# Optimization experiments

Measured on AMD Instinct MI355X. Metric: run time of the kernel, lower is better.

## Reference

```python
import jax, jax.numpy as jnp
import numpy as np

B = 32768      # batch
N_IN = 128     # input nodes
L = 8          # topological layers
W = 256        # nodes per layer
K = 16         # fan-in per node


def setup_inputs() -> dict:
    key = jax.random.key(0)
    k_x, k_w, k_b, k_e = jax.random.split(key, 4)
    inputs = jax.random.normal(k_x, (B, N_IN), dtype=jnp.float32)
    # scale weights down so sigmoid isn't saturated with fan-in 16
    weights = jax.random.normal(k_w, (L, W, K), dtype=jnp.float32) * 0.25
    biases = jax.random.normal(k_b, (L, W), dtype=jnp.float32) * 0.1
    # DAG-valid edges: layer l may only gather from the N_IN + l*W already-computed nodes
    ek = jax.random.split(k_e, L)
    edge_idx = jnp.stack([
        jax.random.randint(ek[l], (W, K), 0, N_IN + l * W, dtype=jnp.int32)
        for l in range(L)
    ])  # [L, W, K]
    return {"inputs": inputs, "weights": weights, "biases": biases,
            "edge_idx": edge_idx}


def reference(inputs, weights, biases, edge_idx):
    # values buffer starts as the input-node activations: [B, N_IN]
    vals = inputs
    n_layers = weights.shape[0]
    for l in range(n_layers):
        gathered = vals[:, edge_idx[l]]                      # [B, W, K] per-node gather
        pre = jnp.einsum('bwk,wk->bw', gathered, weights[l]) + biases[l]
        vals = jnp.concatenate([vals, jax.nn.sigmoid(pre)], axis=1)
    # output nodes are the last layer, concatenated in order
    return vals[:, -W:]
```

## Files before the change

kernel.cpp:

```cpp
#include <hip/hip_runtime.h>
#include <hip/hip_bf16.h>
#include <hip/hip_fp16.h>


#define NB   32768
#define NIN  128
#define NL   8
#define NW   256
#define NK   16
#define RPB  8
#define STORED (NIN + (NL - 1) * NW)

typedef _Float16 h2 __attribute__((ext_vector_type(2)));
typedef __fp16   fp16v2 __attribute__((ext_vector_type(2)));

__device__ __forceinline__ unsigned pk16(float a, float b) {
    fp16v2 p = __builtin_amdgcn_cvt_pkrtz(a, b);
    return __builtin_bit_cast(unsigned, p);
}

__device__ __forceinline__ void fma_feat(float acc[RPB], float w, uint4 p) {
    const h2 h0 = __builtin_bit_cast(h2, p.x);
    const h2 h1 = __builtin_bit_cast(h2, p.y);
    const h2 h2v = __builtin_bit_cast(h2, p.z);
    const h2 h3 = __builtin_bit_cast(h2, p.w);
    acc[0] = fmaf((float)h0[0], w, acc[0]);
    acc[1] = fmaf((float)h0[1], w, acc[1]);
    acc[2] = fmaf((float)h1[0], w, acc[2]);
    acc[3] = fmaf((float)h1[1], w, acc[3]);
    acc[4] = fmaf((float)h2v[0], w, acc[4]);
    acc[5] = fmaf((float)h2v[1], w, acc[5]);
    acc[6] = fmaf((float)h3[0], w, acc[6]);
    acc[7] = fmaf((float)h3[1], w, acc[7]);
}

__global__ __launch_bounds__(256, 5)
void ffn_gather_kernel(const float* __restrict__ inputs,
                       const float* __restrict__ weights,
                       const float* __restrict__ biases,
                       const int*   __restrict__ edge_idx,
                       float* __restrict__ out)
{
    __shared__ uint4 vals[STORED];

    const int t = threadIdx.x;
    const long long row0 = (long long)blockIdx.x * RPB;

    if (t < NIN) {
        float v[RPB];
        #pragma unroll
        for (int r = 0; r < RPB; ++r) v[r] = inputs[(row0 + r) * NIN + t];
        uint4 p;
        p.x = pk16(v[0], v[1]);
        p.y = pk16(v[2], v[3]);
        p.z = pk16(v[4], v[5]);
        p.w = pk16(v[6], v[7]);
        vals[t] = p;
    }
    __syncthreads();

    #pragma unroll
    for (int l = 0; l < NL; ++l) {
        const int base = (l * NW + t) * NK;
        const int4*   iq = (const int4*)(edge_idx + base);
        const float4* wq = (const float4*)(weights + base);

        const float b = biases[l * NW + t];
        float acc[RPB];
        #pragma unroll
        for (int r = 0; r < RPB; ++r) acc[r] = b;

        #pragma unroll
        for (int kk = 0; kk < NK / 4; ++kk) {
            const int4   i4 = iq[kk];
            const float4 w4 = wq[kk];
            const uint4 p0 = vals[i4.x];
            const uint4 p1 = vals[i4.y];
            const uint4 p2 = vals[i4.z];
            const uint4 p3 = vals[i4.w];
            fma_feat(acc, w4.x, p0);
            fma_feat(acc, w4.y, p1);
            fma_feat(acc, w4.z, p2);
            fma_feat(acc, w4.w, p3);
        }

        float s[RPB];
        #pragma unroll
        for (int r = 0; r < RPB; ++r)
            s[r] = 1.0f / (1.0f + __expf(-acc[r]));

        if (l < NL - 1) {
            uint4 p;
            p.x = pk16(s[0], s[1]);
            p.y = pk16(s[2], s[3]);
            p.z = pk16(s[4], s[5]);
            p.w = pk16(s[6], s[7]);
            vals[NIN + l * NW + t] = p;
            __syncthreads();
        } else {
            #pragma unroll
            for (int r = 0; r < RPB; ++r)
                out[(row0 + r) * NW + t] = s[r];
        }
    }
}

extern "C" void kernel_launch(void* const* d_in, const int* in_sizes, int n_in,
                              void* d_out, int out_size, void* d_ws, size_t ws_size,
                              hipStream_t stream)
{
    const float* inputs   = (const float*)d_in[0];
    const float* weights  = (const float*)d_in[1];
    const float* biases   = (const float*)d_in[2];
    const int*   edge_idx = (const int*)d_in[3];
    float* out = (float*)d_out;

    dim3 grid(NB / RPB);
    dim3 block(NW);
    ffn_gather_kernel<<<grid, block, 0, stream>>>(inputs, weights, biases,
                                                  edge_idx, out);
}
```

Before: 143.8 us.

## Accumulate in packed fp16 with a prepass for byte offsets and packed weights

Replaces the fp32 accumulation of fp16-stored activations with packed half2 FMAs (v_pk_fma_f16), so each weight handles two rows per instruction and the per-element fp16-to-fp32 conversions go away. A small prepass kernel turns edge indices into byte offsets and packs each weight as a duplicated half2 in the workspace, removing the shifts and conversions from the main loop. This gives up fp32 accumulation precision over 16 terms, and adds an extra kernel launch plus workspace traffic. If the workspace is too small, it falls back to converting inline.

```diff
diff --git a/kernel.cpp b/kernel.cpp
--- a/kernel.cpp
+++ b/kernel.cpp
@@ -10,41 +10,41 @@
 #define NK   16
 #define RPB  8
 #define STORED (NIN + (NL - 1) * NW)
+#define NPARAM (NL * NW * NK)
 
-typedef _Float16 h2 __attribute__((ext_vector_type(2)));
-typedef __fp16   fp16v2 __attribute__((ext_vector_type(2)));
+typedef __fp16 fp16v2 __attribute__((ext_vector_type(2)));
 
 __device__ __forceinline__ unsigned pk16(float a, float b) {
     fp16v2 p = __builtin_amdgcn_cvt_pkrtz(a, b);
     return __builtin_bit_cast(unsigned, p);
 }
 
-__device__ __forceinline__ void fma_feat(float acc[RPB], float w, uint4 p) {
-    const h2 h0 = __builtin_bit_cast(h2, p.x);
-    const h2 h1 = __builtin_bit_cast(h2, p.y);
-    const h2 h2v = __builtin_bit_cast(h2, p.z);
-    const h2 h3 = __builtin_bit_cast(h2, p.w);
-    acc[0] = fmaf((float)h0[0], w, acc[0]);
-    acc[1] = fmaf((float)h0[1], w, acc[1]);
-    acc[2] = fmaf((float)h1[0], w, acc[2]);
-    acc[3] = fmaf((float)h1[1], w, acc[3]);
-    acc[4] = fmaf((float)h2v[0], w, acc[4]);
-    acc[5] = fmaf((float)h2v[1], w, acc[5]);
-    acc[6] = fmaf((float)h3[0], w, acc[6]);
-    acc[7] = fmaf((float)h3[1], w, acc[7]);
+__device__ __forceinline__ __half2 as_h2(unsigned u) {
+    return __builtin_bit_cast(__half2, u);
 }
 
+__device__ __forceinline__ void fma_feat(__half2 acc[4], __half2 w2, uint4 p) {
+    acc[0] = __hfma2(as_h2(p.x), w2, acc[0]);
+    acc[1] = __hfma2(as_h2(p.y), w2, acc[1]);
+    acc[2] = __hfma2(as_h2(p.z), w2, acc[2]);
+    acc[3] = __hfma2(as_h2(p.w), w2, acc[3]);
+}
+
+template <bool PRE>
 __global__ __launch_bounds__(256, 5)
 void ffn_gather_kernel(const float* __restrict__ inputs,
                        const float* __restrict__ weights,
                        const float* __restrict__ biases,
                        const int*   __restrict__ edge_idx,
+                       const int*   __restrict__ idxb,
+                       const unsigned* __restrict__ wpk,
                        float* __restrict__ out)
 {
     __shared__ uint4 vals[STORED];
 
     const int t = threadIdx.x;
     const long long row0 = (long long)blockIdx.x * RPB;
+    const char* vbase = (const char*)vals;
 
     if (t < NIN) {
         float v[RPB];
@@ -62,32 +62,48 @@
     #pragma unroll
     for (int l = 0; l < NL; ++l) {
         const int base = (l * NW + t) * NK;
-        const int4*   iq = (const int4*)(edge_idx + base);
-        const float4* wq = (const float4*)(weights + base);
 
         const float b = biases[l * NW + t];
-        float acc[RPB];
+        __half2 acc[4];
+        const __half2 bb = __float2half2_rn(b);
         #pragma unroll
-        for (int r = 0; r < RPB; ++r) acc[r] = b;
+        for (int j = 0; j < 4; ++j) acc[j] = bb;
 
         #pragma unroll
         for (int kk = 0; kk < NK / 4; ++kk) {
-            const int4   i4 = iq[kk];
-            const float4 w4 = wq[kk];
-            const uint4 p0 = vals[i4.x];
-            const uint4 p1 = vals[i4.y];
-            const uint4 p2 = vals[i4.z];
-            const uint4 p3 = vals[i4.w];
-            fma_feat(acc, w4.x, p0);
-            fma_feat(acc, w4.y, p1);
-            fma_feat(acc, w4.z, p2);
-            fma_feat(acc, w4.w, p3);
+            int4 o4;
+            __half2 w0, w1, w2, w3;
+            if (PRE) {
+                o4 = ((const int4*)(idxb + base))[kk];
+                uint4 wp = ((const uint4*)(wpk + base))[kk];
+                w0 = as_h2(wp.x); w1 = as_h2(wp.y);
+                w2 = as_h2(wp.z); w3 = as_h2(wp.w);
+            } else {
+                int4 i4 = ((const int4*)(edge_idx + base))[kk];
+                o4.x = i4.x << 4; o4.y = i4.y << 4;
+                o4.z = i4.z << 4; o4.w = i4.w << 4;
+                float4 w4 = ((const float4*)(weights + base))[kk];
+                w0 = __float2half2_rn(w4.x);
+                w1 = __float2half2_rn(w4.y);
+                w2 = __float2half2_rn(w4.z);
+                w3 = __float2half2_rn(w4.w);
+            }
+            const uint4 p0 = *(const uint4*)(vbase + o4.x);
+            const uint4 p1 = *(const uint4*)(vbase + o4.y);
+            const uint4 p2 = *(const uint4*)(vbase + o4.z);
+            const uint4 p3 = *(const uint4*)(vbase + o4.w);
+            fma_feat(acc, w0, p0);
+            fma_feat(acc, w1, p1);
+            fma_feat(acc, w2, p2);
+            fma_feat(acc, w3, p3);
         }
 
         float s[RPB];
         #pragma unroll
-        for (int r = 0; r < RPB; ++r)
-            s[r] = 1.0f / (1.0f + __expf(-acc[r]));
+        for (int j = 0; j < 4; ++j) {
+            s[2 * j + 0] = 1.0f / (1.0f + __expf(-__low2float(acc[j])));
+            s[2 * j + 1] = 1.0f / (1.0f + __expf(-__high2float(acc[j])));
+        }
 
         if (l < NL - 1) {
             uint4 p;
@@ -105,6 +121,18 @@
     }
 }
 
+__global__ __launch_bounds__(256)
+void prepass_kernel(const float* __restrict__ weights,
+                    const int* __restrict__ edge_idx,
+                    int* __restrict__ idxb,
+                    unsigned* __restrict__ wpk)
+{
+    const int i = blockIdx.x * 256 + threadIdx.x;
+    idxb[i] = edge_idx[i] << 4;
+    const float w = weights[i];
+    wpk[i] = pk16(w, w);
+}
+
 extern "C" void kernel_launch(void* const* d_in, const int* in_sizes, int n_in,
                               void* d_out, int out_size, void* d_ws, size_t ws_size,
                               hipStream_t stream)
@@ -117,6 +145,17 @@
 
     dim3 grid(NB / RPB);
     dim3 block(NW);
-    ffn_gather_kernel<<<grid, block, 0, stream>>>(inputs, weights, biases,
-                                                  edge_idx, out);
+
+    const size_t need = (size_t)NPARAM * 4 * 2;
+    if (ws_size >= need) {
+        int*      idxb = (int*)d_ws;
+        unsigned* wpk  = (unsigned*)((char*)d_ws + (size_t)NPARAM * 4);
+        prepass_kernel<<<NPARAM / 256, 256, 0, stream>>>(weights, edge_idx,
+                                                         idxb, wpk);
+        ffn_gather_kernel<true><<<grid, block, 0, stream>>>(
+            inputs, weights, biases, edge_idx, idxb, wpk, out);
+    } else {
+        ffn_gather_kernel<false><<<grid, block, 0, stream>>>(
+            inputs, weights, biases, edge_idx, nullptr, nullptr, out);
+    }
 }
```

Result: faster. 139.2 us (-3.2%).
